# Optimization experiments

Hardware: AMD Instinct MI355X
Metric: run time of the kernel (lower is better)

Reference implementation:

```python
import jax, jax.numpy as jnp
import numpy as np

STRIDE = 4
NUM_HEADS = 8


def _make_window(x, stride, nh):
    # (B,C,H,W) -> (B, nh, S, S, (H/S)*(W/S), C/nh)
    b, c, h, w = x.shape
    x = x.reshape(b, nh, c // nh, h // stride, stride, w // stride, stride)
    x = x.transpose(0, 1, 4, 6, 3, 5, 2)
    return x.reshape(b, nh, stride, stride, (h // stride) * (w // stride), c // nh)


def _demake_window(x, h, w):
    # (B, nh, S, S, L, dh) -> (B, nh*dh, H, W)
    b, nh, s, _, L, dh = x.shape
    x = x.reshape(b, nh, s, s, h // s, w // s, dh)
    x = x.transpose(0, 1, 6, 4, 2, 5, 3)
    return x.reshape(b, nh * dh, h, w)


def _proj(x, W, bias):
    # 1x1 conv == per-pixel GEMM: (B,C,H,W),(O,C) -> (B,O,H,W)
    return jnp.einsum('bchw,oc->bohw', x, W) + bias[None, :, None, None]


def setup_inputs() -> dict:
    key = jax.random.key(0)
    ks = jax.random.split(key, 12)
    B, C, H, W = 4, 256, 64, 64
    P, V, O = 256, 256, 256  # proj/value/out channels
    inp = {
        'fea_q': jax.random.normal(ks[0], (B, C, H, W), jnp.float32),
        'fea_k': jax.random.normal(ks[1], (B, C, H, W), jnp.float32),
        'fea_v': jax.random.normal(ks[2], (B, V, H, W), jnp.float32),
        'mask_q': (jax.random.uniform(ks[3], (B, 1, H, W)) > 0.5).astype(jnp.float32),
        'mask_k': (jax.random.uniform(ks[4], (B, 1, H, W)) > 0.5).astype(jnp.float32),
        'q_w': jax.random.normal(ks[5], (P, C), jnp.float32) * 0.02,
        'q_b': jnp.zeros((P,), jnp.float32),
        'k_w': jax.random.normal(ks[6], (P, C), jnp.float32) * 0.02,
        'k_b': jnp.zeros((P,), jnp.float32),
        'v_w': jax.random.normal(ks[7], (O, V), jnp.float32) * 0.02,
        'v_b': jnp.zeros((O,), jnp.float32),
    }
    return inp


def reference(fea_q, fea_k, fea_v, mask_q, mask_k, q_w, q_b, k_w, k_b, v_w, v_b):
    B, _, H, W = fea_q.shape
    head_dim = q_w.shape[0] // NUM_HEADS
    scaling = head_dim ** (-0.5)

    query = _make_window(_proj(fea_q, q_w, q_b), STRIDE, NUM_HEADS)
    key = _make_window(_proj(fea_k, k_w, k_b), STRIDE, NUM_HEADS)
    value = _make_window(_proj(fea_v, v_w, v_b), STRIDE, NUM_HEADS)

    # (B, nh, S, S, L, L)
    weights = jnp.matmul(query, jnp.swapaxes(key, -1, -2)) * scaling

    # mask attention (no-grad in original)
    mq = _make_window(jax.lax.stop_gradient(mask_q), STRIDE, 1)
    mk = _make_window(jax.lax.stop_gradient(mask_k), STRIDE, 1)
    mask_attn = jnp.matmul(mq, jnp.swapaxes(mk, -1, -2))  # (B,1,S,S,L,L)
    mask_sum = jnp.sum(mask_attn, axis=-1, keepdims=True)
    mask_attn = mask_attn + (mask_sum == 0).astype(jnp.float32)
    mask_attn = jnp.where(mask_attn == 0, -jnp.inf,
                          jnp.where(mask_attn == 1, 0.0, mask_attn))
    weights = weights + mask_attn

    weights = jax.nn.softmax(weights, axis=-1)  # dropout p=0 -> identity
    weights = weights * (1.0 - (mask_sum == 0).astype(jnp.float32))

    out = jnp.matmul(weights, value)  # (B, nh, S, S, L, dh)
    return _demake_window(out, H, W)
```

## Files before the change

### kernel.cpp

```cpp
#include <hip/hip_runtime.h>
#include <hip/hip_bf16.h>

#define NH 8
#define DH 32
#define LW 256
#define HW 4096
#define CIN 256

typedef float f32x4 __attribute__((ext_vector_type(4)));
typedef short s16x8 __attribute__((ext_vector_type(8)));
typedef short s16x4 __attribute__((ext_vector_type(4)));

#define AS1 __attribute__((address_space(1)))
#define AS3 __attribute__((address_space(3)))

__device__ __forceinline__ short f2bf(float f) {
  __hip_bfloat16 h = __float2bfloat16(f);
  short s; __builtin_memcpy(&s, &h, 2); return s;
}

__device__ __forceinline__ void gload_lds16(const void* g, void* l) {
  __builtin_amdgcn_global_load_lds((const AS1 void*)g, (AS3 void*)l, 16, 0, 0);
}

#define KOFF 4194304
#define VOFF 8388608

__global__ void __launch_bounds__(256, 4)
proj_kernel(const float* __restrict__ fq, const float* __restrict__ fk,
            const float* __restrict__ fv,
            const float* __restrict__ qw, const float* __restrict__ qb,
            const float* __restrict__ kw, const float* __restrict__ kb_,
            const float* __restrict__ vw, const float* __restrict__ vb,
            short* __restrict__ ws) {
  __shared__ s16x8 SMEM[1536];
  s16x8* AsV = SMEM;
  s16x8* BsV = SMEM + 512;

  int bid = blockIdx.x;
  int orig = (bid & 7) * 192 + (bid >> 3);
  int t = orig >> 9;
  int r0 = orig & 511;
  int b = r0 >> 7;
  int pblk = (r0 >> 2) & 31;
  int oblk = r0 & 3;

  const float* fea = (t == 0) ? fq : ((t == 1) ? fk : fv);
  const float* Wm  = (t == 0) ? qw : ((t == 1) ? kw : vw);
  const float* Bv  = (t == 0) ? qb : ((t == 1) ? kb_ : vb);

  int p0 = pblk * 128, o0 = oblk * 64;
  int tid = threadIdx.x;
  int lane = tid & 63, wv = tid >> 6;
  int g = lane >> 4, li = lane & 15;

  const f32x4 fzero = {0.f, 0.f, 0.f, 0.f};
  f32x4 acc[8];
#pragma unroll
  for (int n = 0; n < 8; ++n) acc[n] = fzero;

  const float* feab = fea + b * (CIN * HW);
  int coct = tid >> 5;
  int pq = (tid & 31) * 4;

  f32x4 ldA[4];
  f32x4 ldB[8];

#define LOAD_A(cs_) do { int c0_ = (cs_) * 64; _Pragma("unroll") \
  for (int i_ = 0; i_ < 2; ++i_) { int ch_ = i_ * 256 + tid; int o_ = ch_ >> 3, kb2_ = ch_ & 7; \
    const float* s_ = Wm + (o0 + o_) * CIN + c0_ + kb2_ * 8; \
    ldA[2 * i_] = *(const f32x4*)s_; ldA[2 * i_ + 1] = *(const f32x4*)(s_ + 4); } } while (0)

#define LOAD_B(cs_) do { int c0_ = (cs_) * 64; _Pragma("unroll") \
  for (int j_ = 0; j_ < 8; ++j_) \
    ldB[j_] = *(const f32x4*)(feab + (c0_ + coct * 8 + j_) * HW + p0 + pq); } while (0)

#define WRITE_AB() do { _Pragma("unroll") \
  for (int i_ = 0; i_ < 2; ++i_) { int ch_ = i_ * 256 + tid; int o_ = ch_ >> 3, kb2_ = ch_ & 7; \
    s16x8 v_; _Pragma("unroll") \
    for (int j_ = 0; j_ < 4; ++j_) { v_[j_] = f2bf(ldA[2 * i_][j_]); v_[4 + j_] = f2bf(ldA[2 * i_ + 1][j_]); } \
    AsV[o_ * 8 + (kb2_ ^ (o_ & 7))] = v_; } \
  _Pragma("unroll") \
  for (int pp_ = 0; pp_ < 4; ++pp_) { s16x8 v_; _Pragma("unroll") \
    for (int j_ = 0; j_ < 8; ++j_) v_[j_] = f2bf(ldB[j_][pp_]); \
    int p_ = pq + pp_; int pidx_ = p_ ^ ((p_ >> 3) & 7); \
    BsV[coct * 128 + pidx_] = v_; } } while (0)

  LOAD_A(0);
  LOAD_B(0);

  for (int cs = 0; cs < 4; ++cs) {
    __syncthreads();
    WRITE_AB();
    __syncthreads();
    if (cs < 3) { LOAD_A(cs + 1); LOAD_B(cs + 1); }
#pragma unroll
    for (int kk = 0; kk < 2; ++kk) {
      int or0 = wv * 16 + li;
      s16x8 a0 = AsV[or0 * 8 + ((kk * 4 + g) ^ (or0 & 7))];
#pragma unroll
      for (int n = 0; n < 8; ++n) {
        int p = n * 16 + li;
        int pidx = p ^ ((p >> 3) & 7);
        s16x8 bb = BsV[(kk * 4 + g) * 128 + pidx];
        acc[n] = __builtin_amdgcn_mfma_f32_16x16x32_bf16(a0, bb, acc[n], 0, 0, 0);
      }
    }
  }
#undef LOAD_A
#undef LOAD_B
#undef WRITE_AB

  int od = o0 + wv * 16 + g * 4;
  float bias_r[4];
#pragma unroll
  for (int rr = 0; rr < 4; ++rr) bias_r[rr] = Bv[od + rr];

  if (t != 2) {
    int nh = od >> 5;
    int kb = (od & 31) >> 3;
    int dlo = od & 7;
#pragma unroll
    for (int n = 0; n < 8; ++n) {
      int p = p0 + n * 16 + li;
      int h = p >> 6, w = p & 63;
      int s1 = h & 3, h0 = h >> 2, s2 = w & 3, w0 = w >> 2;
      int wwin = s1 * 4 + s2, l = h0 * 16 + w0;
      int winbase = (b * NH + nh) * 16 + wwin;
      s16x4 v;
#pragma unroll
      for (int rr = 0; rr < 4; ++rr) v[rr] = f2bf(acc[n][rr] + bias_r[rr]);
      short* dst = ws + (t == 0 ? 0 : KOFF);
      *(s16x4*)(dst + winbase * 8192 + (kb * 256 + l) * 8 + dlo) = v;
    }
  } else {
    __syncthreads();
    short* Tr = (short*)SMEM;
    int ob = wv * 16 + g * 4;
#pragma unroll
    for (int n = 0; n < 8; ++n) {
      int p = n * 16 + li;
      s16x4 v;
#pragma unroll
      for (int rr = 0; rr < 4; ++rr) v[rr] = f2bf(acc[n][rr] + bias_r[rr]);
      *(s16x4*)(Tr + p * 64 + (ob ^ ((p & 15) << 2))) = v;
    }
    __syncthreads();
    int o_local = tid >> 2;
    int sub = tid & 3;
    int h_idx = sub >> 1;
    int woct = sub & 1;
    int o = o0 + o_local;
    int nh2 = o >> 5, d = o & 31;
    int hh = (p0 >> 6) + h_idx;
    int s1e = hh & 3, h0e = hh >> 2;
#pragma unroll
    for (int s2e = 0; s2e < 4; ++s2e) {
      s16x8 v;
#pragma unroll
      for (int k = 0; k < 8; ++k) {
        int pl = h_idx * 64 + s2e + 32 * woct + 4 * k;
        v[k] = Tr[pl * 64 + (o_local ^ ((pl & 15) << 2))];
      }
      int wwin = s1e * 4 + s2e;
      int l_oct = h0e * 2 + woct;
      int winbase = (b * NH + nh2) * 16 + wwin;
      *(s16x8*)(ws + VOFF + winbase * 8192 + d * 256 + l_oct * 8) = v;
    }
  }
}

__global__ void __launch_bounds__(256, 4)
attn_kernel(const short* __restrict__ ws, const float* __restrict__ mq,
            const float* __restrict__ mk, float* __restrict__ out) {
  __shared__ s16x8 KsV[1024];
  __shared__ s16x8 PsV[512];
  __shared__ float amaskS[256];
  __shared__ float mqS[128];
  __shared__ float facS[128];
  __shared__ int anyS[4];

  int bid = blockIdx.x;
  int orig = (bid & 7) * 128 + (bid >> 3);
  int qh = orig & 1;
  int s2 = (orig >> 1) & 3, s1 = (orig >> 3) & 3, nh = (orig >> 5) & 7, b = orig >> 8;
  int wwin = s1 * 4 + s2;
  int tid = threadIdx.x;
  int lane = tid & 63, wv = tid >> 6, g = lane >> 4, li = lane & 15;

  int winbase = (b * NH + nh) * 16 + wwin;
  const short* qt = ws + winbase * 8192;
  const short* kt = ws + KOFF + winbase * 8192;
  const short* vt = ws + VOFF + winbase * 8192;

#pragma unroll
  for (int i = 0; i < 4; ++i) {
    int seg = i * 4 + wv;
    gload_lds16(kt + (seg * 64 + lane) * 8, &KsV[seg * 64]);
  }

  {
    int l = tid;
    int h = (l >> 4) * 4 + s1, w = (l & 15) * 4 + s2;
    float mkv = mk[b * HW + h * 64 + w];
    amaskS[l] = (mkv > 0.5f) ? 0.0f : -1e30f;
    unsigned long long bal = __ballot(mkv > 0.5f);
    if (lane == 0) anyS[wv] = (bal != 0ULL) ? 1 : 0;
  }
  if (tid < 128) {
    int l = qh * 128 + tid;
    int h = (l >> 4) * 4 + s1, w = (l & 15) * 4 + s2;
    mqS[tid] = mq[b * HW + h * 64 + w];
  }

  int lq0 = wv * 32;
  s16x8 qa[2];
#pragma unroll
  for (int m = 0; m < 2; ++m)
    qa[m] = *(const s16x8*)(qt + (g * 256 + qh * 128 + lq0 + m * 16 + li) * 8);

  __syncthreads();
  int anyk = anyS[0] | anyS[1] | anyS[2] | anyS[3];

  const f32x4 fzero = {0.f, 0.f, 0.f, 0.f};
  f32x4 of[2][2];
#pragma unroll
  for (int m = 0; m < 2; ++m) { of[m][0] = fzero; of[m][1] = fzero; }
  float rs[8];
#pragma unroll
  for (int i = 0; i < 8; ++i) rs[i] = 0.0f;

  const float C = 0.17677669529663689f * 1.4426950408889634f;

#pragma unroll
  for (int lkb = 0; lkb < 4; ++lkb) {
    f32x4 sa[2][4];
#pragma unroll
    for (int n = 0; n < 4; ++n) {
      s16x8 kf = KsV[g * 256 + lkb * 64 + n * 16 + li];
#pragma unroll
      for (int m = 0; m < 2; ++m)
        sa[m][n] = __builtin_amdgcn_mfma_f32_16x16x32_bf16(qa[m], kf, fzero, 0, 0, 0);
    }
#pragma unroll
    for (int ks = 0; ks < 2; ++ks) {
#pragma unroll
      for (int n2 = 0; n2 < 2; ++n2) {
        int n = ks * 2 + n2;
        float am = amaskS[lkb * 64 + n * 16 + li];
#pragma unroll
        for (int m = 0; m < 2; ++m) {
#pragma unroll
          for (int rr = 0; rr < 4; ++rr) {
            float pval = exp2f(sa[m][n][rr] * C + am);
            rs[m * 4 + rr] += pval;
            int row = m * 16 + g * 4 + rr;
            int cl = n * 16 + li;
            int kbh = (cl >> 3) & 3;
            short* ps = (short*)&PsV[wv * 128 + kbh * 32 + row];
            ps[cl & 7] = f2bf(pval);
          }
        }
      }
      int kg = lkb * 2 + ks;
      s16x8 pb[2];
#pragma unroll
      for (int n = 0; n < 2; ++n) pb[n] = PsV[wv * 128 + g * 32 + n * 16 + li];
#pragma unroll
      for (int m2 = 0; m2 < 2; ++m2) {
        s16x8 va = *(const s16x8*)(vt + (m2 * 16 + li) * 256 + (kg * 4 + g) * 8);
#pragma unroll
        for (int n = 0; n < 2; ++n)
          of[m2][n] = __builtin_amdgcn_mfma_f32_16x16x32_bf16(va, pb[n], of[m2][n], 0, 0, 0);
      }
    }
  }

#pragma unroll
  for (int i = 0; i < 8; ++i) {
    float v = rs[i];
    v += __shfl_xor(v, 1);
    v += __shfl_xor(v, 2);
    v += __shfl_xor(v, 4);
    v += __shfl_xor(v, 8);
    rs[i] = v;
  }
  if (li == 0) {
#pragma unroll
    for (int m = 0; m < 2; ++m)
#pragma unroll
      for (int rr = 0; rr < 4; ++rr) {
        int row = m * 16 + g * 4 + rr;
        float sum = rs[m * 4 + rr];
        facS[wv * 32 + row] = (anyk && mqS[wv * 32 + row] > 0.5f) ? (1.0f / sum) : 0.0f;
      }
  }

#pragma unroll
  for (int m2 = 0; m2 < 2; ++m2) {
#pragma unroll
    for (int n = 0; n < 2; ++n) {
      int lloc = wv * 32 + n * 16;
      float fac = facS[lloc + li];
      int l = qh * 128 + lloc;
      int h = (l >> 4) * 4 + s1;
      int w = li * 4 + s2;
#pragma unroll
      for (int rr = 0; rr < 4; ++rr) {
        int o = nh * 32 + m2 * 16 + g * 4 + rr;
        out[((b * 256 + o) * 64 + h) * 64 + w] = of[m2][n][rr] * fac;
      }
    }
  }
}

extern "C" void kernel_launch(void* const* d_in, const int* in_sizes, int n_in,
                              void* d_out, int out_size, void* d_ws, size_t ws_size,
                              hipStream_t stream) {
  const float* fq = (const float*)d_in[0];
  const float* fk = (const float*)d_in[1];
  const float* fv = (const float*)d_in[2];
  const float* mq = (const float*)d_in[3];
  const float* mk = (const float*)d_in[4];
  const float* qw = (const float*)d_in[5];
  const float* qb = (const float*)d_in[6];
  const float* kw = (const float*)d_in[7];
  const float* kb = (const float*)d_in[8];
  const float* vw = (const float*)d_in[9];
  const float* vb = (const float*)d_in[10];
  short* ws = (short*)d_ws;

  proj_kernel<<<1536, 256, 0, stream>>>(fq, fk, fv, qw, qb, kw, kb, vw, vb, ws);
  attn_kernel<<<1024, 256, 0, stream>>>(ws, mq, mk, (float*)d_out);
}
```

Before: 48.70 us.

## Pre-convert features and weights to swizzled bf16, stage via async LDS loads

Adds a prep kernel that converts the fp32 input features and projection weights once into bf16 tiles already laid out in the swizzled LDS order. The projection GEMM then streams those tiles into a double-buffered LDS ring with global_load_lds, instead of loading fp32, converting and writing LDS in registers. The aim is to stop each of the four output-channel blocks re-reading and re-converting the same fp32 features, and to overlap loads with MFMA. The cost is an extra kernel launch plus a full bf16 copy of the inputs written to and read back from the workspace.

```diff
diff --git a/kernel.cpp b/kernel.cpp
--- a/kernel.cpp
+++ b/kernel.cpp
@@ -25,17 +25,65 @@
 
 #define KOFF 4194304
 #define VOFF 8388608
+#define FBOFF 12582912
+#define WT2OFF 25165824
 
 __global__ void __launch_bounds__(256, 4)
-proj_kernel(const float* __restrict__ fq, const float* __restrict__ fk,
+prep_kernel(const float* __restrict__ fq, const float* __restrict__ fk,
             const float* __restrict__ fv,
-            const float* __restrict__ qw, const float* __restrict__ qb,
-            const float* __restrict__ kw, const float* __restrict__ kb_,
-            const float* __restrict__ vw, const float* __restrict__ vb,
-            short* __restrict__ ws) {
-  __shared__ s16x8 SMEM[1536];
-  s16x8* AsV = SMEM;
-  s16x8* BsV = SMEM + 512;
+            const float* __restrict__ qw, const float* __restrict__ kw,
+            const float* __restrict__ vw, short* __restrict__ ws) {
+  int blk = blockIdx.x;
+  int tid = threadIdx.x;
+  if (blk < 384) {
+    int t = blk >> 7, b = (blk >> 5) & 3, pblk = blk & 31;
+    const float* fea = (t == 0) ? fq : ((t == 1) ? fk : fv);
+    const float* feab = fea + b * (CIN * HW);
+    short* dstblk = ws + FBOFF + (((t * 4 + b) * 32 + pblk)) * 32768;
+    int coct = tid >> 5, pq = (tid & 31) * 4;
+#pragma unroll
+    for (int cs = 0; cs < 4; ++cs) {
+      f32x4 ld[8];
+#pragma unroll
+      for (int j = 0; j < 8; ++j)
+        ld[j] = *(const f32x4*)(feab + (cs * 64 + coct * 8 + j) * HW + pblk * 128 + pq);
+#pragma unroll
+      for (int pp = 0; pp < 4; ++pp) {
+        s16x8 v;
+#pragma unroll
+        for (int j = 0; j < 8; ++j) v[j] = f2bf(ld[j][pp]);
+        int p = pq + pp;
+        int pidx = p ^ ((p >> 3) & 7);
+        *(s16x8*)(dstblk + ((cs * 8 + coct) * 128 + pidx) * 8) = v;
+      }
+    }
+  } else {
+    int idx = blk - 384;
+    int t = idx >> 2, oblk = idx & 3, o0 = oblk * 64;
+    const float* Wm = (t == 0) ? qw : ((t == 1) ? kw : vw);
+    short* wdst = ws + WT2OFF + idx * 16384;
+#pragma unroll
+    for (int cs = 0; cs < 4; ++cs) {
+#pragma unroll
+      for (int i = 0; i < 2; ++i) {
+        int ch = i * 256 + tid;
+        int o = ch >> 3, kb2 = ch & 7;
+        const float* src = Wm + (o0 + o) * CIN + cs * 64 + kb2 * 8;
+        f32x4 w0 = *(const f32x4*)(src);
+        f32x4 w1 = *(const f32x4*)(src + 4);
+        s16x8 v;
+#pragma unroll
+        for (int j = 0; j < 4; ++j) { v[j] = f2bf(w0[j]); v[4 + j] = f2bf(w1[j]); }
+        *(s16x8*)(wdst + cs * 4096 + (o * 8 + (kb2 ^ (o & 7))) * 8) = v;
+      }
+    }
+  }
+}
+
+__global__ void __launch_bounds__(256, 3)
+proj_kernel(const float* __restrict__ qb, const float* __restrict__ kb_,
+            const float* __restrict__ vb, short* __restrict__ ws) {
+  __shared__ s16x8 SMEM[3072];
 
   int bid = blockIdx.x;
   int orig = (bid & 7) * 192 + (bid >> 3);
@@ -45,76 +93,69 @@
   int pblk = (r0 >> 2) & 31;
   int oblk = r0 & 3;
 
-  const float* fea = (t == 0) ? fq : ((t == 1) ? fk : fv);
-  const float* Wm  = (t == 0) ? qw : ((t == 1) ? kw : vw);
-  const float* Bv  = (t == 0) ? qb : ((t == 1) ? kb_ : vb);
+  const float* Bv = (t == 0) ? qb : ((t == 1) ? kb_ : vb);
 
   int p0 = pblk * 128, o0 = oblk * 64;
   int tid = threadIdx.x;
   int lane = tid & 63, wv = tid >> 6;
   int g = lane >> 4, li = lane & 15;
 
+  const short* feaBblk = ws + FBOFF + ((t * 4 + b) * 32 + pblk) * 32768;
+  const short* wtblk   = ws + WT2OFF + (t * 4 + oblk) * 16384;
+
   const f32x4 fzero = {0.f, 0.f, 0.f, 0.f};
   f32x4 acc[8];
 #pragma unroll
   for (int n = 0; n < 8; ++n) acc[n] = fzero;
 
-  const float* feab = fea + b * (CIN * HW);
-  int coct = tid >> 5;
-  int pq = (tid & 31) * 4;
-
-  f32x4 ldA[4];
-  f32x4 ldB[8];
-
-#define LOAD_A(cs_) do { int c0_ = (cs_) * 64; _Pragma("unroll") \
-  for (int i_ = 0; i_ < 2; ++i_) { int ch_ = i_ * 256 + tid; int o_ = ch_ >> 3, kb2_ = ch_ & 7; \
-    const float* s_ = Wm + (o0 + o_) * CIN + c0_ + kb2_ * 8; \
-    ldA[2 * i_] = *(const f32x4*)s_; ldA[2 * i_ + 1] = *(const f32x4*)(s_ + 4); } } while (0)
-
-#define LOAD_B(cs_) do { int c0_ = (cs_) * 64; _Pragma("unroll") \
-  for (int j_ = 0; j_ < 8; ++j_) \
-    ldB[j_] = *(const f32x4*)(feab + (c0_ + coct * 8 + j_) * HW + p0 + pq); } while (0)
-
-#define WRITE_AB() do { _Pragma("unroll") \
-  for (int i_ = 0; i_ < 2; ++i_) { int ch_ = i_ * 256 + tid; int o_ = ch_ >> 3, kb2_ = ch_ & 7; \
-    s16x8 v_; _Pragma("unroll") \
-    for (int j_ = 0; j_ < 4; ++j_) { v_[j_] = f2bf(ldA[2 * i_][j_]); v_[4 + j_] = f2bf(ldA[2 * i_ + 1][j_]); } \
-    AsV[o_ * 8 + (kb2_ ^ (o_ & 7))] = v_; } \
-  _Pragma("unroll") \
-  for (int pp_ = 0; pp_ < 4; ++pp_) { s16x8 v_; _Pragma("unroll") \
-    for (int j_ = 0; j_ < 8; ++j_) v_[j_] = f2bf(ldB[j_][pp_]); \
-    int p_ = pq + pp_; int pidx_ = p_ ^ ((p_ >> 3) & 7); \
-    BsV[coct * 128 + pidx_] = v_; } } while (0)
-
-  LOAD_A(0);
-  LOAD_B(0);
-
+  int od = o0 + wv * 16 + g * 4;
+  float bias_r[4];
+#pragma unroll
+  for (int rr = 0; rr < 4; ++rr) bias_r[rr] = Bv[od + rr];
+  asm volatile("s_waitcnt vmcnt(0)" ::: "memory");
+  __builtin_amdgcn_sched_barrier(0);
+
+#define STAGE(cs_, buf_) do { \
+    const short* as_ = wtblk + (cs_) * 4096; \
+    s16x8* ad_ = SMEM + (buf_) * 1536; \
+    _Pragma("unroll") \
+    for (int i_ = 0; i_ < 2; ++i_) { int seg_ = i_ * 4 + wv; \
+      gload_lds16(as_ + (seg_ * 64 + lane) * 8, ad_ + seg_ * 64); } \
+    const short* bs_ = feaBblk + (cs_) * 8192; \
+    s16x8* bd_ = SMEM + (buf_) * 1536 + 512; \
+    _Pragma("unroll") \
+    for (int i_ = 0; i_ < 4; ++i_) { int seg_ = i_ * 4 + wv; \
+      gload_lds16(bs_ + (seg_ * 64 + lane) * 8, bd_ + seg_ * 64); } } while (0)
+
+  STAGE(0, 0);
+
+#pragma unroll
   for (int cs = 0; cs < 4; ++cs) {
-    __syncthreads();
-    WRITE_AB();
-    __syncthreads();
-    if (cs < 3) { LOAD_A(cs + 1); LOAD_B(cs + 1); }
+    if (cs < 3) STAGE(cs + 1, (cs + 1) & 1);
+    if (cs < 3) { asm volatile("s_waitcnt vmcnt(6)" ::: "memory"); }
+    else        { asm volatile("s_waitcnt vmcnt(0)" ::: "memory"); }
+    __builtin_amdgcn_sched_barrier(0);
+    __builtin_amdgcn_s_barrier();
+    __builtin_amdgcn_sched_barrier(0);
+    const s16x8* Abuf = SMEM + (cs & 1) * 1536;
+    const s16x8* Bbuf = Abuf + 512;
 #pragma unroll
     for (int kk = 0; kk < 2; ++kk) {
       int or0 = wv * 16 + li;
-      s16x8 a0 = AsV[or0 * 8 + ((kk * 4 + g) ^ (or0 & 7))];
+      s16x8 a0 = Abuf[or0 * 8 + ((kk * 4 + g) ^ (or0 & 7))];
 #pragma unroll
       for (int n = 0; n < 8; ++n) {
         int p = n * 16 + li;
         int pidx = p ^ ((p >> 3) & 7);
-        s16x8 bb = BsV[(kk * 4 + g) * 128 + pidx];
+        s16x8 bb = Bbuf[(kk * 4 + g) * 128 + pidx];
         acc[n] = __builtin_amdgcn_mfma_f32_16x16x32_bf16(a0, bb, acc[n], 0, 0, 0);
       }
     }
-  }
-#undef LOAD_A
-#undef LOAD_B
-#undef WRITE_AB
-
-  int od = o0 + wv * 16 + g * 4;
-  float bias_r[4];
-#pragma unroll
-  for (int rr = 0; rr < 4; ++rr) bias_r[rr] = Bv[od + rr];
+    __builtin_amdgcn_sched_barrier(0);
+    __builtin_amdgcn_s_barrier();
+    __builtin_amdgcn_sched_barrier(0);
+  }
+#undef STAGE
 
   if (t != 2) {
     int nh = od >> 5;
@@ -134,7 +175,6 @@
       *(s16x4*)(dst + winbase * 8192 + (kb * 256 + l) * 8 + dlo) = v;
     }
   } else {
-    __syncthreads();
     short* Tr = (short*)SMEM;
     int ob = wv * 16 + g * 4;
 #pragma unroll
@@ -330,6 +370,7 @@
   const float* vb = (const float*)d_in[10];
   short* ws = (short*)d_ws;
 
-  proj_kernel<<<1536, 256, 0, stream>>>(fq, fk, fv, qw, qb, kw, kb, vw, vb, ws);
+  prep_kernel<<<396, 256, 0, stream>>>(fq, fk, fv, qw, kw, vw, ws);
+  proj_kernel<<<1536, 256, 0, stream>>>(qb, kb, vb, ws);
   attn_kernel<<<1024, 256, 0, stream>>>(ws, mq, mk, (float*)d_out);
 }
```

New measurement: 56.25 us. 15.5% more time.
